# Kernel optimization log

Measured on AMD Instinct MI355X. Metric: run time of the kernel, lower is better.

Reference implementation:

```python
import jax, jax.numpy as jnp
import numpy as np

N_EXPERTS = 20
DIM = 32
EPS = 1e-12  # F.normalize eps


def setup_inputs() -> dict:
    key = jax.random.key(0)
    k_x, k_pos, k_w1, k_b1, k_w0, k_b0 = jax.random.split(key, 6)
    B = 131072
    bound = 1.0 / np.sqrt(DIM)  # torch Linear default init range
    return {
        "x": jax.random.normal(k_x, (B, DIM), dtype=jnp.float32),
        "W1": jax.random.uniform(k_w1, (N_EXPERTS, DIM, DIM), jnp.float32, -bound, bound),
        "b1": jax.random.uniform(k_b1, (N_EXPERTS, DIM), jnp.float32, -bound, bound),
        "W0": jax.random.uniform(k_w0, (N_EXPERTS, DIM, DIM), jnp.float32, -bound, bound),
        "b0": jax.random.uniform(k_b0, (N_EXPERTS, DIM), jnp.float32, -bound, bound),
        "pos": jax.random.randint(k_pos, (B,), 0, N_EXPERTS, dtype=jnp.int64),
    }


def reference(x, W1, b1, W0, b0, pos):
    # Gather per-sample expert weights (routing): [B, DIM, DIM] / [B, DIM]
    W1g, b1g = W1[pos], b1[pos]
    W0g, b0g = W0[pos], b0[pos]
    # fc1: y = x @ W1^T + b1 (torch Linear convention, W is [out, in])
    h = jnp.einsum("bi,boi->bo", x, W1g) + b1g
    # fc0
    out = jnp.einsum("bi,boi->bo", h, W0g) + b0g
    # F.normalize(dim=-1): x / max(||x||_2, eps)
    norm = jnp.sqrt(jnp.sum(out * out, axis=-1, keepdims=True))
    return out / jnp.maximum(norm, EPS)
```

## Files before the change

kernel.cpp:

```cpp
#include <hip/hip_runtime.h>
#include <stdint.h>

#define N_EXPERTS 20
#define DIM 32
#define TMOE 512
#define MSTR 1032

static __device__ __forceinline__ short f2bf(float f) {
    union { float f; uint32_t u; } v; v.f = f;
    uint32_t u = v.u;
    return (short)(uint16_t)((u + 0x7FFFu + ((u >> 16) & 1u)) >> 16);
}
static __device__ __forceinline__ float bfl(uint32_t u) {
    union { uint32_t u; float f; } v; v.u = u << 16; return v.f;
}
static __device__ __forceinline__ float bfh(uint32_t u) {
    union { uint32_t u; float f; } v; v.u = u & 0xFFFF0000u; return v.f;
}

__global__ __launch_bounds__(256) void k_prep(
    const float* __restrict__ W1, const float* __restrict__ b1,
    const float* __restrict__ W0, const float* __restrict__ b0,
    unsigned short* __restrict__ Mbf, float* __restrict__ cvec)
{
    __shared__ float s1[1024], s0[1024];
    int e = blockIdx.x, t = threadIdx.x;
    const float* w1 = W1 + e * 1024;
    const float* w0 = W0 + e * 1024;
    for (int i = t; i < 1024; i += 256) { s1[i] = w1[i]; s0[i] = w0[i]; }
    __syncthreads();
    for (int idx = t; idx < 1024; idx += 256) {
        int o = idx >> 5, i = idx & 31;
        float s = 0.f;
        #pragma unroll
        for (int k = 0; k < 32; k++) s += s0[o*32 + k] * s1[k*32 + i];
        Mbf[e*1024 + o*32 + i] = (unsigned short)f2bf(s);
    }
    if (t < DIM) {
        float s = b0[e*32 + t];
        #pragma unroll
        for (int k = 0; k < 32; k++) s += s0[t*32 + k] * b1[e*32 + k];
        cvec[e*32 + t] = s;
    }
}

__global__ __launch_bounds__(TMOE) void k_moe(
    const float* __restrict__ x, const int* __restrict__ pos,
    const unsigned short* __restrict__ Mbf, const float* __restrict__ cvec,
    float* __restrict__ out, int B)
{
    __shared__ unsigned short Ms[N_EXPERTS * MSTR];
    __shared__ float cs[N_EXPERTS * DIM];

    int t = threadIdx.x;
    int s = blockIdx.x * TMOE + t;

    float4 xv[8];
    int e = 0;
    bool live = (s < B);
    if (live) {
        const float4* xp = (const float4*)(x + (size_t)s * 32);
        #pragma unroll
        for (int i = 0; i < 8; i++) xv[i] = xp[i];
        e = pos[s];
    }

    {
        const uint4* msrc = (const uint4*)Mbf;
        for (int i = t; i < N_EXPERTS * 128; i += TMOE) {
            int ee = i >> 7, r = i & 127;
            uint4 v = msrc[i];
            *(uint4*)&Ms[ee * MSTR + r * 8] = v;
        }
        for (int i = t; i < N_EXPERTS * DIM; i += TMOE) cs[i] = cvec[i];
    }
    __syncthreads();
    if (!live) return;

    const unsigned short* M = Ms + e * MSTR;
    const float* c = cs + e * 32;

    float acc[32];
    #pragma unroll 4
    for (int o = 0; o < 32; o++) {
        const uint4* mp = (const uint4*)(M + o * 32);
        float a = c[o];
        #pragma unroll
        for (int kk = 0; kk < 4; kk++) {
            uint4 m = mp[kk];
            float4 x0 = xv[2*kk], x1 = xv[2*kk + 1];
            a += bfl(m.x) * x0.x + bfh(m.x) * x0.y
               + bfl(m.y) * x0.z + bfh(m.y) * x0.w
               + bfl(m.z) * x1.x + bfh(m.z) * x1.y
               + bfl(m.w) * x1.z + bfh(m.w) * x1.w;
        }
        acc[o] = a;
    }

    float ss = 0.f;
    #pragma unroll
    for (int o = 0; o < 32; o++) ss += acc[o] * acc[o];
    float sc = rsqrtf(fmaxf(ss, 1e-24f));

    float4* op = (float4*)(out + (size_t)s * 32);
    #pragma unroll
    for (int k = 0; k < 8; k++) {
        float4 v;
        v.x = acc[4*k + 0] * sc;
        v.y = acc[4*k + 1] * sc;
        v.z = acc[4*k + 2] * sc;
        v.w = acc[4*k + 3] * sc;
        op[k] = v;
    }
}

extern "C" void kernel_launch(void* const* d_in, const int* in_sizes, int n_in,
                              void* d_out, int out_size, void* d_ws, size_t ws_size,
                              hipStream_t stream) {
    const float* x  = (const float*)d_in[0];
    const float* W1 = (const float*)d_in[1];
    const float* b1 = (const float*)d_in[2];
    const float* W0 = (const float*)d_in[3];
    const float* b0 = (const float*)d_in[4];
    const int*  pos = (const int*)d_in[5];
    float* out = (float*)d_out;
    int B = in_sizes[0] / DIM;

    char* ws = (char*)d_ws;
    unsigned short* Mbf = (unsigned short*)ws;
    float* cvec = (float*)(ws + (size_t)N_EXPERTS * 1024 * 2);

    k_prep<<<N_EXPERTS, 256, 0, stream>>>(W1, b1, W0, b0, Mbf, cvec);
    int nblk = (B + TMOE - 1) / TMOE;
    k_moe<<<nblk, TMOE, 0, stream>>>(x, pos, Mbf, cvec, out, B);
}
```

Measured before the change: 90.41 us.

## Fuse expert weight folding into main kernel using per-block MFMA

Drops the separate prep kernel and has every block recompute the folded W0·W1 matrices and bias vectors for all experts with bf16 MFMA instructions, writing them straight into shared memory. This removes one kernel launch and the global workspace round trip between the two kernels. In exchange each of the 256 blocks repeats the fold (40 wave tasks reading W0/W1 from global/L2), and W1 and b1 are now rounded to bf16 before the product, which loses some precision. The bias vector is read as float4 with a padded stride, and the output loop is now fully unrolled.

```diff
diff --git a/kernel.cpp b/kernel.cpp
--- a/kernel.cpp
+++ b/kernel.cpp
@@ -5,6 +5,10 @@
 #define DIM 32
 #define TMOE 512
 #define MSTR 1032
+#define CSTR 36
+
+using frag_ab = __attribute__((ext_vector_type(8))) short;
+using frag_cd = __attribute__((ext_vector_type(4))) float;
 
 static __device__ __forceinline__ short f2bf(float f) {
     union { float f; uint32_t u; } v; v.f = f;
@@ -18,42 +22,19 @@
     union { uint32_t u; float f; } v; v.u = u & 0xFFFF0000u; return v.f;
 }
 
-__global__ __launch_bounds__(256) void k_prep(
+__global__ __launch_bounds__(TMOE) void k_moe(
+    const float* __restrict__ x, const int* __restrict__ pos,
     const float* __restrict__ W1, const float* __restrict__ b1,
     const float* __restrict__ W0, const float* __restrict__ b0,
-    unsigned short* __restrict__ Mbf, float* __restrict__ cvec)
-{
-    __shared__ float s1[1024], s0[1024];
-    int e = blockIdx.x, t = threadIdx.x;
-    const float* w1 = W1 + e * 1024;
-    const float* w0 = W0 + e * 1024;
-    for (int i = t; i < 1024; i += 256) { s1[i] = w1[i]; s0[i] = w0[i]; }
-    __syncthreads();
-    for (int idx = t; idx < 1024; idx += 256) {
-        int o = idx >> 5, i = idx & 31;
-        float s = 0.f;
-        #pragma unroll
-        for (int k = 0; k < 32; k++) s += s0[o*32 + k] * s1[k*32 + i];
-        Mbf[e*1024 + o*32 + i] = (unsigned short)f2bf(s);
-    }
-    if (t < DIM) {
-        float s = b0[e*32 + t];
-        #pragma unroll
-        for (int k = 0; k < 32; k++) s += s0[t*32 + k] * b1[e*32 + k];
-        cvec[e*32 + t] = s;
-    }
-}
-
-__global__ __launch_bounds__(TMOE) void k_moe(
-    const float* __restrict__ x, const int* __restrict__ pos,
-    const unsigned short* __restrict__ Mbf, const float* __restrict__ cvec,
     float* __restrict__ out, int B)
 {
     __shared__ unsigned short Ms[N_EXPERTS * MSTR];
-    __shared__ float cs[N_EXPERTS * DIM];
+    __shared__ float cs[N_EXPERTS * CSTR];
 
     int t = threadIdx.x;
     int s = blockIdx.x * TMOE + t;
+    int lane = t & 63, wave = t >> 6;
+    int n = lane & 15, q = lane >> 4;
 
     float4 xv[8];
     int e = 0;
@@ -65,26 +46,65 @@
         e = pos[s];
     }
 
-    {
-        const uint4* msrc = (const uint4*)Mbf;
-        for (int i = t; i < N_EXPERTS * 128; i += TMOE) {
-            int ee = i >> 7, r = i & 127;
-            uint4 v = msrc[i];
-            *(uint4*)&Ms[ee * MSTR + r * 8] = v;
+    #pragma unroll 1
+    for (int task = wave; task < 2 * N_EXPERTS; task += TMOE / 64) {
+        int te = task >> 1, r = task & 1;
+        const float* w0 = W0 + te * 1024;
+        const float* w1 = W1 + te * 1024;
+
+        const float* ap = w0 + (16 * r + n) * 32 + q * 8;
+        float4 a0 = *(const float4*)ap;
+        float4 a1 = *(const float4*)(ap + 4);
+        frag_ab af;
+        af[0]=f2bf(a0.x); af[1]=f2bf(a0.y); af[2]=f2bf(a0.z); af[3]=f2bf(a0.w);
+        af[4]=f2bf(a1.x); af[5]=f2bf(a1.y); af[6]=f2bf(a1.z); af[7]=f2bf(a1.w);
+
+        frag_ab bf0, bf1, bb;
+        #pragma unroll
+        for (int j = 0; j < 8; j++) {
+            int k = q * 8 + j;
+            bf0[j] = f2bf(w1[k * 32 + n]);
+            bf1[j] = f2bf(w1[k * 32 + 16 + n]);
+            short bv = f2bf(b1[te * 32 + k]);
+            bb[j] = (n == 0) ? bv : (short)0;
         }
-        for (int i = t; i < N_EXPERTS * DIM; i += TMOE) cs[i] = cvec[i];
+        frag_cd z = {0.f, 0.f, 0.f, 0.f};
+        frag_cd d0 = __builtin_amdgcn_mfma_f32_16x16x32_bf16(af, bf0, z, 0, 0, 0);
+        frag_cd d1 = __builtin_amdgcn_mfma_f32_16x16x32_bf16(af, bf1, z, 0, 0, 0);
+        frag_cd dc = __builtin_amdgcn_mfma_f32_16x16x32_bf16(af, bb, z, 0, 0, 0);
+
+        unsigned short* mrow = Ms + te * MSTR;
+        #pragma unroll
+        for (int reg = 0; reg < 4; reg++) {
+            int row = 16 * r + q * 4 + reg;
+            mrow[row * 32 + n]      = (unsigned short)f2bf(d0[reg]);
+            mrow[row * 32 + 16 + n] = (unsigned short)f2bf(d1[reg]);
+        }
+        if (n == 0) {
+            #pragma unroll
+            for (int reg = 0; reg < 4; reg++) {
+                int row = 16 * r + q * 4 + reg;
+                cs[te * CSTR + row] = dc[reg] + b0[te * 32 + row];
+            }
+        }
     }
     __syncthreads();
     if (!live) return;
 
     const unsigned short* M = Ms + e * MSTR;
-    const float* c = cs + e * 32;
+    const float4* cp = (const float4*)(cs + e * CSTR);
 
     float acc[32];
-    #pragma unroll 4
+    #pragma unroll
+    for (int g = 0; g < 8; g++) {
+        float4 cv = cp[g];
+        acc[4*g+0] = cv.x; acc[4*g+1] = cv.y; acc[4*g+2] = cv.z; acc[4*g+3] = cv.w;
+    }
+
+    #pragma unroll
     for (int o = 0; o < 32; o++) {
         const uint4* mp = (const uint4*)(M + o * 32);
-        float a = c[o];
+        float a = acc[o];
         #pragma unroll
         for (int kk = 0; kk < 4; kk++) {
             uint4 m = mp[kk];
@@ -104,13 +124,13 @@
 
     float4* op = (float4*)(out + (size_t)s * 32);
     #pragma unroll
-    for (int k = 0; k < 8; k++) {
+    for (int g = 0; g < 8; g++) {
         float4 v;
-        v.x = acc[4*k + 0] * sc;
-        v.y = acc[4*k + 1] * sc;
-        v.z = acc[4*k + 2] * sc;
-        v.w = acc[4*k + 3] * sc;
-        op[k] = v;
+        v.x = acc[4*g+0] * sc;
+        v.y = acc[4*g+1] * sc;
+        v.z = acc[4*g+2] * sc;
+        v.w = acc[4*g+3] * sc;
+        op[g] = v;
     }
 }
 
@@ -126,11 +146,6 @@
     float* out = (float*)d_out;
     int B = in_sizes[0] / DIM;
 
-    char* ws = (char*)d_ws;
-    unsigned short* Mbf = (unsigned short*)ws;
-    float* cvec = (float*)(ws + (size_t)N_EXPERTS * 1024 * 2);
-
-    k_prep<<<N_EXPERTS, 256, 0, stream>>>(W1, b1, W0, b0, Mbf, cvec);
     int nblk = (B + TMOE - 1) / TMOE;
-    k_moe<<<nblk, TMOE, 0, stream>>>(x, pos, Mbf, cvec, out, B);
+    k_moe<<<nblk, TMOE, 0, stream>>>(x, pos, W1, b1, W0, b0, out, B);
 }
```

After: 91.90 us. About the same (+1.7%).
